# Performance work log

Hardware: AMD Instinct MI355X
Metric: run time of the kernel (lower is better)

The kernel has to match this reference:

```python
import jax, jax.numpy as jnp
import numpy as np

B, S_IMG, S_TXT, D, H, HD, R = 1, 1536, 512, 3072, 24, 128, 32
INNER = H * HD  # 3072
EPS = 1e-5


def svdq_linear(x, W, down, up, b=None):
    # Float reference of SVDQW4A4Linear: quantized base GEMM + SVD low-rank branch.
    y = x @ W.T + (x @ down) @ up
    if b is not None:
        y = y + b
    return y


def rms_norm(x, w):
    # RMSNorm over last dim (dim_head)
    var = jnp.mean(x * x, axis=-1, keepdims=True)
    return x * jax.lax.rsqrt(var + EPS) * w


def apply_rope(x, cos, sin):
    # x: (B, S, H, HD); cos/sin: (S, HD//2), interleaved complex rotation
    b, s, h, d = x.shape
    xr = x.reshape(b, s, h, d // 2, 2)
    x0, x1 = xr[..., 0], xr[..., 1]
    c = cos[None, :, None, :]
    sn = sin[None, :, None, :]
    o0 = x0 * c - x1 * sn
    o1 = x0 * sn + x1 * c
    return jnp.stack([o0, o1], axis=-1).reshape(b, s, h, d)


def setup_inputs() -> dict:
    key = jax.random.key(0)
    ks = jax.random.split(key, 24)
    sc = 0.02
    inp = {
        'hidden_states': jax.random.normal(ks[0], (B, S_IMG, D), jnp.float32),
        'encoder_hidden_states': jax.random.normal(ks[1], (B, S_TXT, D), jnp.float32),
    }
    S = S_IMG + S_TXT
    theta = jax.random.uniform(ks[2], (S, HD // 2), jnp.float32, 0.0, 2.0 * np.pi)
    inp['rope_cos'] = jnp.cos(theta)
    inp['rope_sin'] = jnp.sin(theta)
    inp['qkv_w'] = jax.random.normal(ks[3], (3 * INNER, D), jnp.float32) * sc
    inp['qkv_down'] = jax.random.normal(ks[4], (D, R), jnp.float32) * sc
    inp['qkv_up'] = jax.random.normal(ks[5], (R, 3 * INNER), jnp.float32) * sc
    inp['add_qkv_w'] = jax.random.normal(ks[6], (3 * INNER, D), jnp.float32) * sc
    inp['add_qkv_down'] = jax.random.normal(ks[7], (D, R), jnp.float32) * sc
    inp['add_qkv_up'] = jax.random.normal(ks[8], (R, 3 * INNER), jnp.float32) * sc
    inp['out_w'] = jax.random.normal(ks[9], (D, INNER), jnp.float32) * sc
    inp['out_down'] = jax.random.normal(ks[10], (INNER, R), jnp.float32) * sc
    inp['out_up'] = jax.random.normal(ks[11], (R, D), jnp.float32) * sc
    inp['out_b'] = jnp.zeros((D,), jnp.float32)
    inp['add_out_w'] = jax.random.normal(ks[12], (D, INNER), jnp.float32) * sc
    inp['add_out_down'] = jax.random.normal(ks[13], (INNER, R), jnp.float32) * sc
    inp['add_out_up'] = jax.random.normal(ks[14], (R, D), jnp.float32) * sc
    inp['add_out_b'] = jnp.zeros((D,), jnp.float32)
    inp['norm_q_w'] = jnp.ones((HD,), jnp.float32)
    inp['norm_k_w'] = jnp.ones((HD,), jnp.float32)
    inp['norm_added_q_w'] = jnp.ones((HD,), jnp.float32)
    inp['norm_added_k_w'] = jnp.ones((HD,), jnp.float32)
    return inp


def reference(hidden_states, encoder_hidden_states, rope_cos, rope_sin,
              qkv_w, qkv_down, qkv_up,
              add_qkv_w, add_qkv_down, add_qkv_up,
              out_w, out_down, out_up, out_b,
              add_out_w, add_out_down, add_out_up, add_out_b,
              norm_q_w, norm_k_w, norm_added_q_w, norm_added_k_w):
    seq_txt = encoder_hidden_states.shape[1]

    img_qkv = svdq_linear(hidden_states, qkv_w, qkv_down, qkv_up)
    img_q, img_k, img_v = jnp.split(img_qkv, 3, axis=-1)
    txt_qkv = svdq_linear(encoder_hidden_states, add_qkv_w, add_qkv_down, add_qkv_up)
    txt_q, txt_k, txt_v = jnp.split(txt_qkv, 3, axis=-1)

    def heads(x):
        return x.reshape(x.shape[0], x.shape[1], H, HD)

    img_q, img_k, img_v = heads(img_q), heads(img_k), heads(img_v)
    txt_q, txt_k, txt_v = heads(txt_q), heads(txt_k), heads(txt_v)

    img_q = rms_norm(img_q, norm_q_w)
    img_k = rms_norm(img_k, norm_k_w)
    txt_q = rms_norm(txt_q, norm_added_q_w)
    txt_k = rms_norm(txt_k, norm_added_k_w)

    q = jnp.concatenate([txt_q, img_q], axis=1)  # (B, S, H, HD)
    k = jnp.concatenate([txt_k, img_k], axis=1)
    v = jnp.concatenate([txt_v, img_v], axis=1)

    q = apply_rope(q, rope_cos, rope_sin)
    k = apply_rope(k, rope_cos, rope_sin)

    scale = 1.0 / jnp.sqrt(jnp.asarray(HD, q.dtype))
    scores = jnp.einsum('bqhd,bkhd->bhqk', q, k) * scale
    probs = jax.nn.softmax(scores, axis=-1)
    attn = jnp.einsum('bhqk,bkhd->bqhd', probs, v)
    attn = attn.reshape(attn.shape[0], attn.shape[1], INNER)

    txt_attn = attn[:, :seq_txt, :]
    img_attn = attn[:, seq_txt:, :]

    img_out = svdq_linear(img_attn, out_w, out_down, out_up, out_b)
    txt_out = svdq_linear(txt_attn, add_out_w, add_out_down, add_out_up, add_out_b)
    return (img_out, txt_out)
```

## Files before the change

kernel.cpp:

```cpp
#include <hip/hip_runtime.h>
#include <hip/hip_bf16.h>
#include <stdint.h>

typedef __hip_bfloat16 bf16;
typedef __attribute__((ext_vector_type(8))) short short8;
typedef __attribute__((ext_vector_type(4))) short short4b;
typedef __attribute__((ext_vector_type(4))) float floatx4;

__device__ __forceinline__ short bfs(float x) {
    uint32_t u = __builtin_bit_cast(uint32_t, x);
    u += 0x7FFFu + ((u >> 16) & 1u);
    return (short)(u >> 16);
}
__device__ __forceinline__ float b2f(bf16 x) { return __bfloat162float(x); }

__device__ __forceinline__ void load_lds16(const bf16* g, bf16* l) {
    __builtin_amdgcn_global_load_lds(
        (const __attribute__((address_space(1))) uint32_t*)g,
        (__attribute__((address_space(3))) uint32_t*)l, 16, 0, 0);
}

__global__ __launch_bounds__(256) void cvt_bf16(const float* __restrict__ X,
                                                bf16* __restrict__ Y) {
    const size_t i = ((size_t)blockIdx.x * 256 + threadIdx.x) * 8;
    const float4 v0 = *(const float4*)(X + i);
    const float4 v1 = *(const float4*)(X + i + 4);
    short8 o = { bfs(v0.x), bfs(v0.y), bfs(v0.z), bfs(v0.w),
                 bfs(v1.x), bfs(v1.y), bfs(v1.z), bfs(v1.w) };
    *(short8*)(Y + i) = o;
}

__global__ __launch_bounds__(64) void transposeR(const float* __restrict__ U,
                                                 bf16* __restrict__ UT, int N) {
    const int n = blockIdx.x * 64 + threadIdx.x;
    #pragma unroll
    for (int r = 0; r < 32; ++r)
        UT[(size_t)n * 32 + r] = __float2bfloat16(U[(size_t)r * N + n]);
}

__global__ __launch_bounds__(256) void downproj(const bf16* __restrict__ X,
                                                const float* __restrict__ Dn,
                                                bf16* __restrict__ T, int K) {
    const int m = blockIdx.x;
    const int n = threadIdx.x & 31;
    const int kg = threadIdx.x >> 5;
    const bf16* x = X + (size_t)m * K;
    const int kc = K >> 3;
    float acc = 0.f;
    #pragma unroll 4
    for (int k = kg * kc; k < (kg + 1) * kc; ++k)
        acc += b2f(x[k]) * Dn[(size_t)k * 32 + n];
    __shared__ float red[8][32];
    red[kg][n] = acc;
    __syncthreads();
    if (threadIdx.x < 32) {
        float s = 0.f;
        #pragma unroll
        for (int g = 0; g < 8; ++g) s += red[g][n];
        T[(size_t)m * 32 + n] = __float2bfloat16(s);
    }
}

__global__ __launch_bounds__(256) void gemm128(
    const bf16* __restrict__ A0, const bf16* __restrict__ B0,
    const bf16* __restrict__ T0, const bf16* __restrict__ U0,
    const bf16* __restrict__ A1, const bf16* __restrict__ B1,
    const bf16* __restrict__ T1, const bf16* __restrict__ U1,
    const float* __restrict__ bias0, const float* __restrict__ bias1,
    float* __restrict__ C0, float* __restrict__ C1,
    bf16* __restrict__ Qb, bf16* __restrict__ Kb, bf16* __restrict__ Vb,
    int mtiles0, int N, int K, int sb0, int sb1, int mode)
{
    __shared__ __align__(16) bf16 As[2][128 * 32];
    __shared__ __align__(16) bf16 Bs[2][128 * 32];
    const int tid = threadIdx.x;
    const int lane = tid & 63, w = tid >> 6;
    const int wm = (w >> 1) * 64, wn = (w & 1) * 64;
    const int lr = lane & 15, lq = lane >> 4;

    int bid = blockIdx.y * gridDim.x + blockIdx.x;
    const int cpx = (gridDim.x * gridDim.y) >> 3;
    bid = (bid & 7) * cpx + (bid >> 3);
    const int by = bid / gridDim.x, bx = bid - by * gridDim.x;

    const bool set1 = (by >= mtiles0);
    const int lby = set1 ? (by - mtiles0) : by;
    const int m0 = lby * 128, n0 = bx * 128;
    const bf16* Asel = set1 ? A1 : A0;
    const bf16* Bsel = set1 ? B1 : B0;
    const bf16* Tsel = set1 ? T1 : T0;
    const bf16* Usel = set1 ? U1 : U0;
    const int s_base = set1 ? sb1 : sb0;

    const int ksteps = K >> 5;

    auto stage = [&](int buf, int kt) {
        const bf16 *a_src, *b_src;
        int lda, ldb;
        if (kt < ksteps) {
            a_src = Asel + (size_t)m0 * K + kt * 32; lda = K;
            b_src = Bsel + (size_t)n0 * K + kt * 32; ldb = K;
        } else {
            a_src = Tsel + (size_t)m0 * 32; lda = 32;
            b_src = Usel + (size_t)n0 * 32; ldb = 32;
        }
        bf16* Ad = &As[buf][0];
        bf16* Bd = &Bs[buf][0];
        #pragma unroll
        for (int it = 0; it < 2; ++it) {
            const int c = tid + it * 256;
            const int row = c >> 2, sub = c & 3;
            load_lds16(a_src + (size_t)row * lda + sub * 8, Ad + c * 8);
        }
        #pragma unroll
        for (int it = 0; it < 2; ++it) {
            const int c = tid + it * 256;
            const int row = c >> 2, sub = c & 3;
            load_lds16(b_src + (size_t)row * ldb + sub * 8, Bd + c * 8);
        }
    };

    floatx4 acc[4][4] = {};
    stage(0, 0);
    __syncthreads();
    int cur = 0;
    for (int kt = 0; kt <= ksteps; ++kt) {
        if (kt < ksteps) stage(cur ^ 1, kt + 1);
        const bf16* Ac = &As[cur][0];
        const bf16* Bc = &Bs[cur][0];
        short8 af[4], bfr[4];
        #pragma unroll
        for (int i = 0; i < 4; ++i)
            af[i] = *(const short8*)(Ac + (wm + i * 16 + lr) * 32 + lq * 8);
        #pragma unroll
        for (int j = 0; j < 4; ++j)
            bfr[j] = *(const short8*)(Bc + (wn + j * 16 + lr) * 32 + lq * 8);
        #pragma unroll
        for (int i = 0; i < 4; ++i)
            #pragma unroll
            for (int j = 0; j < 4; ++j)
                acc[i][j] = __builtin_amdgcn_mfma_f32_16x16x32_bf16(
                    af[i], bfr[j], acc[i][j], 0, 0, 0);
        __syncthreads();
        cur ^= 1;
    }

    if (mode == 0) {
        float* Csel = set1 ? C1 : C0;
        const float* bsel = set1 ? bias1 : bias0;
        #pragma unroll
        for (int j = 0; j < 4; ++j) {
            const int col = n0 + wn + j * 16 + lr;
            const float bv = bsel ? bsel[col] : 0.0f;
            #pragma unroll
            for (int i = 0; i < 4; ++i) {
                const int rowb = m0 + wm + i * 16 + lq * 4;
                #pragma unroll
                for (int r = 0; r < 4; ++r)
                    Csel[(size_t)(rowb + r) * N + col] = acc[i][j][r] + bv;
            }
        }
    } else {
        #pragma unroll
        for (int j = 0; j < 4; ++j) {
            const int col = n0 + wn + j * 16 + lr;
            const int which = col / 3072;
            const int cc = col - which * 3072;
            const int hh = cc >> 7, dd = cc & 127;
            #pragma unroll
            for (int i = 0; i < 4; ++i) {
                const int rowb = m0 + wm + i * 16 + lq * 4;
                const int s0 = s_base + rowb;
                if (which == 2) {
                    short4b pv = { bfs(acc[i][j][0]), bfs(acc[i][j][1]),
                                   bfs(acc[i][j][2]), bfs(acc[i][j][3]) };
                    *(short4b*)(Vb + ((size_t)hh * 128 + dd) * 2048 + s0) = pv;
                } else {
                    bf16* dst = (which == 0 ? Qb : Kb)
                              + ((size_t)hh * 2048 + s0) * 128 + dd;
                    #pragma unroll
                    for (int r = 0; r < 4; ++r)
                        dst[(size_t)r * 128] = __float2bfloat16(acc[i][j][r]);
                }
            }
        }
    }
}

__global__ __launch_bounds__(256) void rmsrope(
    bf16* __restrict__ Qb, bf16* __restrict__ Kb,
    const float* __restrict__ cosb, const float* __restrict__ sinb,
    const float* __restrict__ nqw, const float* __restrict__ nkw,
    const float* __restrict__ naqw, const float* __restrict__ nakw)
{
    const int idx = blockIdx.x * 4 + (threadIdx.x >> 6);
    const int i = threadIdx.x & 63;
    const int s = idx & 2047;
    const int h = idx >> 11;
    const float c  = cosb[s * 64 + i];
    const float sn = sinb[s * 64 + i];
    const bool txt = (s < 512);
    const size_t base = ((size_t)h * 2048 + s) * 128;

    {
        __hip_bfloat162* row = (__hip_bfloat162*)(Qb + base);
        __hip_bfloat162 pv = row[i];
        float x0 = b2f(pv.x), x1 = b2f(pv.y);
        float ss = x0 * x0 + x1 * x1;
        #pragma unroll
        for (int m = 1; m < 64; m <<= 1) ss += __shfl_xor(ss, m);
        const float rms = rsqrtf(ss * (1.0f / 128.0f) + 1e-5f);
        const float2 nw = *(const float2*)((txt ? naqw : nqw) + 2 * i);
        const float y0 = x0 * rms * nw.x;
        const float y1 = x1 * rms * nw.y;
        __hip_bfloat162 o;
        o.x = __float2bfloat16(y0 * c - y1 * sn);
        o.y = __float2bfloat16(y0 * sn + y1 * c);
        row[i] = o;
    }
    {
        __hip_bfloat162* row = (__hip_bfloat162*)(Kb + base);
        __hip_bfloat162 pv = row[i];
        float x0 = b2f(pv.x), x1 = b2f(pv.y);
        float ss = x0 * x0 + x1 * x1;
        #pragma unroll
        for (int m = 1; m < 64; m <<= 1) ss += __shfl_xor(ss, m);
        const float rms = rsqrtf(ss * (1.0f / 128.0f) + 1e-5f);
        const float2 nw = *(const float2*)((txt ? nakw : nkw) + 2 * i);
        const float y0 = x0 * rms * nw.x;
        const float y1 = x1 * rms * nw.y;
        __hip_bfloat162 o;
        o.x = __float2bfloat16(y0 * c - y1 * sn);
        o.y = __float2bfloat16(y0 * sn + y1 * c);
        row[i] = o;
    }
}

__global__ __launch_bounds__(256) void attn64(
    const bf16* __restrict__ Qb, const bf16* __restrict__ Kb,
    const bf16* __restrict__ Vb, bf16* __restrict__ attnb)
{
    __shared__ __align__(16) bf16 Ks[64 * 128];
    __shared__ __align__(16) bf16 VsT[128 * 64];
    __shared__ __align__(16) bf16 Ps[4][16 * 64];
    const int tid = threadIdx.x, lane = tid & 63, w = tid >> 6;
    const int lr = lane & 15, lq = lane >> 4;
    const int h = blockIdx.y, q0 = blockIdx.x * 64;
    const float scale = 0.08838834764831845f;

    const bf16* qrow = Qb + ((size_t)h * 2048 + q0 + w * 16 + lr) * 128;
    short8 qf[4];
    #pragma unroll
    for (int ks = 0; ks < 4; ++ks)
        qf[ks] = *(const short8*)(qrow + ks * 32 + lq * 8);

    floatx4 oacc[8] = {};
    float mrow[4] = {-1e30f, -1e30f, -1e30f, -1e30f};
    float lrow[4] = {0.f, 0.f, 0.f, 0.f};

    for (int kt = 0; kt < 32; ++kt) {
        const int kv0 = kt * 64;
        __syncthreads();
        #pragma unroll
        for (int it = 0; it < 4; ++it) {
            const int c = tid + it * 256;
            const int row = c >> 4, cg = (c & 15) ^ (row & 7);
            load_lds16(Kb + ((size_t)h * 2048 + kv0 + row) * 128 + cg * 8,
                       Ks + c * 8);
        }
        #pragma unroll
        for (int it = 0; it < 4; ++it) {
            const int c = tid + it * 256;
            const int row = c >> 3, cg = (c & 7) ^ (row & 7);
            load_lds16(Vb + ((size_t)h * 128 + row) * 2048 + kv0 + cg * 8,
                       VsT + c * 8);
        }
        __syncthreads();

        floatx4 sacc[4] = {};
        __builtin_amdgcn_s_setprio(1);
        #pragma unroll
        for (int ks = 0; ks < 4; ++ks)
            #pragma unroll
            for (int jt = 0; jt < 4; ++jt) {
                const int row = jt * 16 + lr;
                short8 kf = *(const short8*)(
                    Ks + row * 128 + (((ks * 4 + lq) ^ (row & 7)) * 8));
                sacc[jt] = __builtin_amdgcn_mfma_f32_16x16x32_bf16(qf[ks], kf, sacc[jt], 0, 0, 0);
            }
        __builtin_amdgcn_s_setprio(0);

        float alpha_r[4];
        #pragma unroll
        for (int r = 0; r < 4; ++r) {
            float s0 = sacc[0][r] * scale, s1 = sacc[1][r] * scale;
            float s2 = sacc[2][r] * scale, s3 = sacc[3][r] * scale;
            float mx = fmaxf(fmaxf(s0, s1), fmaxf(s2, s3));
            #pragma unroll
            for (int msk = 1; msk < 16; msk <<= 1)
                mx = fmaxf(mx, __shfl_xor(mx, msk));
            const float mn = fmaxf(mrow[r], mx);
            const float al = __expf(mrow[r] - mn);
            s0 = __expf(s0 - mn); s1 = __expf(s1 - mn);
            s2 = __expf(s2 - mn); s3 = __expf(s3 - mn);
            float sum = s0 + s1 + s2 + s3;
            #pragma unroll
            for (int msk = 1; msk < 16; msk <<= 1)
                sum += __shfl_xor(sum, msk);
            lrow[r] = lrow[r] * al + sum;
            mrow[r] = mn;
            alpha_r[r] = al;
            sacc[0][r] = s0; sacc[1][r] = s1; sacc[2][r] = s2; sacc[3][r] = s3;
        }
        #pragma unroll
        for (int nt = 0; nt < 8; ++nt)
            #pragma unroll
            for (int r = 0; r < 4; ++r) oacc[nt][r] *= alpha_r[r];

        #pragma unroll
        for (int jt = 0; jt < 4; ++jt)
            #pragma unroll
            for (int r = 0; r < 4; ++r) {
                const int q = lq * 4 + r;
                const int ir = jt * 16 + lr;
                Ps[w][q * 64 + ((((ir >> 3) ^ (q & 7))) << 3) + (ir & 7)] =
                    __float2bfloat16(sacc[jt][r]);
            }

        short8 pf[2];
        #pragma unroll
        for (int k2 = 0; k2 < 2; ++k2)
            pf[k2] = *(const short8*)(
                &Ps[w][lr * 64 + (((k2 * 4 + lq) ^ (lr & 7)) << 3)]);
        __builtin_amdgcn_s_setprio(1);
        #pragma unroll
        for (int k2 = 0; k2 < 2; ++k2)
            #pragma unroll
            for (int nt = 0; nt < 8; ++nt) {
                const int row = nt * 16 + lr;
                short8 vf = *(const short8*)(
                    VsT + row * 64 + (((k2 * 4 + lq) ^ (row & 7)) * 8));
                oacc[nt] = __builtin_amdgcn_mfma_f32_16x16x32_bf16(pf[k2], vf, oacc[nt], 0, 0, 0);
            }
        __builtin_amdgcn_s_setprio(0);
    }

    float rl[4];
    #pragma unroll
    for (int r = 0; r < 4; ++r) rl[r] = 1.0f / lrow[r];
    #pragma unroll
    for (int nt = 0; nt < 8; ++nt) {
        const int col = h * 128 + nt * 16 + lr;
        #pragma unroll
        for (int r = 0; r < 4; ++r) {
            const int s = q0 + w * 16 + lq * 4 + r;
            attnb[(size_t)s * 3072 + col] = __float2bfloat16(oacc[nt][r] * rl[r]);
        }
    }
}

extern "C" void kernel_launch(void* const* d_in, const int* in_sizes, int n_in,
                              void* d_out, int out_size, void* d_ws, size_t ws_size,
                              hipStream_t stream)
{
    (void)in_sizes; (void)n_in; (void)out_size; (void)ws_size;
    const float* hs        = (const float*)d_in[0];
    const float* ehs       = (const float*)d_in[1];
    const float* rc        = (const float*)d_in[2];
    const float* rs        = (const float*)d_in[3];
    const float* qkv_w     = (const float*)d_in[4];
    const float* qkv_down  = (const float*)d_in[5];
    const float* qkv_up    = (const float*)d_in[6];
    const float* aqkv_w    = (const float*)d_in[7];
    const float* aqkv_down = (const float*)d_in[8];
    const float* aqkv_up   = (const float*)d_in[9];
    const float* out_w     = (const float*)d_in[10];
    const float* out_down  = (const float*)d_in[11];
    const float* out_up    = (const float*)d_in[12];
    const float* out_b     = (const float*)d_in[13];
    const float* aout_w    = (const float*)d_in[14];
    const float* aout_down = (const float*)d_in[15];
    const float* aout_up   = (const float*)d_in[16];
    const float* aout_b    = (const float*)d_in[17];
    const float* nqw  = (const float*)d_in[18];
    const float* nkw  = (const float*)d_in[19];
    const float* naqw = (const float*)d_in[20];
    const float* nakw = (const float*)d_in[21];

    char* ws = (char*)d_ws;
    size_t o = 0;
    bf16* Qb = (bf16*)(ws + o); o += (size_t)24 * 2048 * 128 * 2;
    bf16* Kb = (bf16*)(ws + o); o += (size_t)24 * 2048 * 128 * 2;
    bf16* Vb = (bf16*)(ws + o); o += (size_t)24 * 2048 * 128 * 2;
    bf16* attnb = (bf16*)(ws + o); o += (size_t)2048 * 3072 * 2;
    bf16* Xbi = (bf16*)(ws + o); o += (size_t)1536 * 3072 * 2;
    bf16* Xbt = (bf16*)(ws + o); o += (size_t)512 * 3072 * 2;
    bf16* Wq  = (bf16*)(ws + o); o += (size_t)9216 * 3072 * 2;
    bf16* Waq = (bf16*)(ws + o); o += (size_t)9216 * 3072 * 2;
    bf16* Wo  = Wq;
    bf16* Wao = Wq + (size_t)3072 * 3072;
    bf16* t_img  = (bf16*)(ws + o); o += (size_t)1536 * 32 * 2;
    bf16* t_txt  = (bf16*)(ws + o); o += (size_t)512 * 32 * 2;
    bf16* t2_img = (bf16*)(ws + o); o += (size_t)1536 * 32 * 2;
    bf16* t2_txt = (bf16*)(ws + o); o += (size_t)512 * 32 * 2;
    bf16* upTq  = (bf16*)(ws + o); o += (size_t)9216 * 32 * 2;
    bf16* upTaq = (bf16*)(ws + o); o += (size_t)9216 * 32 * 2;
    bf16* upTo  = (bf16*)(ws + o); o += (size_t)3072 * 32 * 2;
    bf16* upTao = (bf16*)(ws + o); o += (size_t)3072 * 32 * 2;

    cvt_bf16<<<2304, 256, 0, stream>>>(hs, Xbi);
    cvt_bf16<<<768, 256, 0, stream>>>(ehs, Xbt);
    cvt_bf16<<<13824, 256, 0, stream>>>(qkv_w, Wq);
    cvt_bf16<<<13824, 256, 0, stream>>>(aqkv_w, Waq);

    transposeR<<<144, 64, 0, stream>>>(qkv_up, upTq, 9216);
    transposeR<<<144, 64, 0, stream>>>(aqkv_up, upTaq, 9216);
    transposeR<<<48, 64, 0, stream>>>(out_up, upTo, 3072);
    transposeR<<<48, 64, 0, stream>>>(aout_up, upTao, 3072);
    downproj<<<1536, 256, 0, stream>>>(Xbi, qkv_down, t_img, 3072);
    downproj<<<512, 256, 0, stream>>>(Xbt, aqkv_down, t_txt, 3072);

    gemm128<<<dim3(72, 16), 256, 0, stream>>>(
        Xbi, Wq, t_img, upTq,
        Xbt, Waq, t_txt, upTaq,
        nullptr, nullptr, nullptr, nullptr,
        Qb, Kb, Vb, 12, 9216, 3072, 512, 0, 1);

    cvt_bf16<<<4608, 256, 0, stream>>>(out_w, Wo);
    cvt_bf16<<<4608, 256, 0, stream>>>(aout_w, Wao);

    rmsrope<<<12288, 256, 0, stream>>>(Qb, Kb, rc, rs, nqw, nkw, naqw, nakw);

    attn64<<<dim3(32, 24), 256, 0, stream>>>(Qb, Kb, Vb, attnb);

    downproj<<<1536, 256, 0, stream>>>(attnb + (size_t)512 * 3072, out_down, t2_img, 3072);
    downproj<<<512, 256, 0, stream>>>(attnb, aout_down, t2_txt, 3072);

    float* outp = (float*)d_out;
    gemm128<<<dim3(24, 16), 256, 0, stream>>>(
        attnb + (size_t)512 * 3072, Wo, t2_img, upTo,
        attnb,                      Wao, t2_txt, upTao,
        out_b, aout_b, outp, outp + (size_t)1536 * 3072,
        nullptr, nullptr, nullptr, 12, 3072, 3072, 0, 0, 0);
}
```

Before: 953.9 us.

## Widen GEMM K-tile to 64 with swizzled LDS and interleaved staging phases

The GEMM main loop now steps K by 64 instead of 32, which halves the number of loop iterations and barriers. LDS tiles use an XOR swizzle on the column groups to avoid bank conflicts. The next-tile global-to-LDS loads are split into four parts, each interleaved with one row-block of MFMAs and separated by s_barrier/sched_barrier, with setprio raised around the MFMAs. The low-rank buffers are zero-padded to a rank of 64 so the extra LoRA step fits the 64-wide tile, at the cost of doubled LDS usage and some wasted MFMA work on the padding.

```diff
diff --git a/kernel.cpp b/kernel.cpp
--- a/kernel.cpp
+++ b/kernel.cpp
@@ -19,6 +19,9 @@
         (const __attribute__((address_space(1))) uint32_t*)g,
         (__attribute__((address_space(3))) uint32_t*)l, 16, 0, 0);
 }
+
+#define PHASE_BARRIER() do { __builtin_amdgcn_s_barrier(); \
+                             __builtin_amdgcn_sched_barrier(0); } while (0)
 
 __global__ __launch_bounds__(256) void cvt_bf16(const float* __restrict__ X,
                                                 bf16* __restrict__ Y) {
@@ -34,8 +37,10 @@
                                                  bf16* __restrict__ UT, int N) {
     const int n = blockIdx.x * 64 + threadIdx.x;
     #pragma unroll
-    for (int r = 0; r < 32; ++r)
-        UT[(size_t)n * 32 + r] = __float2bfloat16(U[(size_t)r * N + n]);
+    for (int r = 0; r < 32; ++r) {
+        UT[(size_t)n * 64 + r] = __float2bfloat16(U[(size_t)r * N + n]);
+        UT[(size_t)n * 64 + 32 + r] = __float2bfloat16(0.0f);
+    }
 }
 
 __global__ __launch_bounds__(256) void downproj(const bf16* __restrict__ X,
@@ -57,11 +62,12 @@
         float s = 0.f;
         #pragma unroll
         for (int g = 0; g < 8; ++g) s += red[g][n];
-        T[(size_t)m * 32 + n] = __float2bfloat16(s);
-    }
-}
-
-__global__ __launch_bounds__(256) void gemm128(
+        T[(size_t)m * 64 + n] = __float2bfloat16(s);
+        T[(size_t)m * 64 + 32 + n] = __float2bfloat16(0.0f);
+    }
+}
+
+__global__ __launch_bounds__(256) void gemm64k(
     const bf16* __restrict__ A0, const bf16* __restrict__ B0,
     const bf16* __restrict__ T0, const bf16* __restrict__ U0,
     const bf16* __restrict__ A1, const bf16* __restrict__ B1,
@@ -71,8 +77,8 @@
     bf16* __restrict__ Qb, bf16* __restrict__ Kb, bf16* __restrict__ Vb,
     int mtiles0, int N, int K, int sb0, int sb1, int mode)
 {
-    __shared__ __align__(16) bf16 As[2][128 * 32];
-    __shared__ __align__(16) bf16 Bs[2][128 * 32];
+    __shared__ __align__(16) bf16 As[2][128 * 64];
+    __shared__ __align__(16) bf16 Bs[2][128 * 64];
     const int tid = threadIdx.x;
     const int lane = tid & 63, w = tid >> 6;
     const int wm = (w >> 1) * 64, wn = (w & 1) * 64;
@@ -92,57 +98,90 @@
     const bf16* Usel = set1 ? U1 : U0;
     const int s_base = set1 ? sb1 : sb0;
 
-    const int ksteps = K >> 5;
-
-    auto stage = [&](int buf, int kt) {
-        const bf16 *a_src, *b_src;
-        int lda, ldb;
-        if (kt < ksteps) {
-            a_src = Asel + (size_t)m0 * K + kt * 32; lda = K;
-            b_src = Bsel + (size_t)n0 * K + kt * 32; ldb = K;
-        } else {
-            a_src = Tsel + (size_t)m0 * 32; lda = 32;
-            b_src = Usel + (size_t)n0 * 32; ldb = 32;
-        }
-        bf16* Ad = &As[buf][0];
-        bf16* Bd = &Bs[buf][0];
+    const int ksteps = K >> 6;
+
+    auto stageA = [&](int buf, int kt, int part) {
+        const bf16* src; int ld;
+        if (kt < ksteps) { src = Asel + (size_t)m0 * K + kt * 64; ld = K; }
+        else             { src = Tsel + (size_t)m0 * 64;          ld = 64; }
+        bf16* dst = &As[buf][0];
         #pragma unroll
         for (int it = 0; it < 2; ++it) {
-            const int c = tid + it * 256;
-            const int row = c >> 2, sub = c & 3;
-            load_lds16(a_src + (size_t)row * lda + sub * 8, Ad + c * 8);
-        }
+            const int c = tid + part * 512 + it * 256;
+            const int row = c >> 3, cg = (c & 7) ^ (row & 7);
+            load_lds16(src + (size_t)row * ld + cg * 8, dst + c * 8);
+        }
+    };
+    auto stageB = [&](int buf, int kt, int part) {
+        const bf16* src; int ld;
+        if (kt < ksteps) { src = Bsel + (size_t)n0 * K + kt * 64; ld = K; }
+        else             { src = Usel + (size_t)n0 * 64;          ld = 64; }
+        bf16* dst = &Bs[buf][0];
         #pragma unroll
         for (int it = 0; it < 2; ++it) {
-            const int c = tid + it * 256;
-            const int row = c >> 2, sub = c & 3;
-            load_lds16(b_src + (size_t)row * ldb + sub * 8, Bd + c * 8);
+            const int c = tid + part * 512 + it * 256;
+            const int row = c >> 3, cg = (c & 7) ^ (row & 7);
+            load_lds16(src + (size_t)row * ld + cg * 8, dst + c * 8);
         }
     };
 
     floatx4 acc[4][4] = {};
-    stage(0, 0);
+    short8 bfr[4][2];
+
+    stageA(0, 0, 0); stageA(0, 0, 1);
+    stageB(0, 0, 0); stageB(0, 0, 1);
     __syncthreads();
-    int cur = 0;
+
     for (int kt = 0; kt <= ksteps; ++kt) {
-        if (kt < ksteps) stage(cur ^ 1, kt + 1);
-        const bf16* Ac = &As[cur][0];
-        const bf16* Bc = &Bs[cur][0];
-        short8 af[4], bfr[4];
-        #pragma unroll
-        for (int i = 0; i < 4; ++i)
-            af[i] = *(const short8*)(Ac + (wm + i * 16 + lr) * 32 + lq * 8);
-        #pragma unroll
-        for (int j = 0; j < 4; ++j)
-            bfr[j] = *(const short8*)(Bc + (wn + j * 16 + lr) * 32 + lq * 8);
-        #pragma unroll
-        for (int i = 0; i < 4; ++i)
-            #pragma unroll
-            for (int j = 0; j < 4; ++j)
-                acc[i][j] = __builtin_amdgcn_mfma_f32_16x16x32_bf16(
-                    af[i], bfr[j], acc[i][j], 0, 0, 0);
+        const int buf = kt & 1, nbuf = buf ^ 1;
+        const bool more = (kt < ksteps);
+        const bf16* Ac = &As[buf][0];
+        const bf16* Bc = &Bs[buf][0];
+
+        auto readA = [&](int p, short8 af[2]) {
+            const int row = wm + p * 16 + lr;
+            #pragma unroll
+            for (int k2 = 0; k2 < 2; ++k2)
+                af[k2] = *(const short8*)(
+                    Ac + row * 64 + (((k2 * 4 + lq) ^ (row & 7)) << 3));
+        };
+        auto mfmaP = [&](int p, short8 af[2]) {
+            __builtin_amdgcn_s_setprio(1);
+            #pragma unroll
+            for (int k2 = 0; k2 < 2; ++k2)
+                #pragma unroll
+                for (int j = 0; j < 4; ++j)
+                    acc[p][j] = __builtin_amdgcn_mfma_f32_16x16x32_bf16(
+                        af[k2], bfr[j][k2], acc[p][j], 0, 0, 0);
+            __builtin_amdgcn_s_setprio(0);
+        };
+
+        short8 af[2];
+        #pragma unroll
+        for (int j = 0; j < 4; ++j) {
+            const int row = wn + j * 16 + lr;
+            #pragma unroll
+            for (int k2 = 0; k2 < 2; ++k2)
+                bfr[j][k2] = *(const short8*)(
+                    Bc + row * 64 + (((k2 * 4 + lq) ^ (row & 7)) << 3));
+        }
+        readA(0, af);
+        if (more) stageA(nbuf, kt + 1, 0);
+        PHASE_BARRIER();
+        mfmaP(0, af);
+        readA(1, af);
+        if (more) stageA(nbuf, kt + 1, 1);
+        PHASE_BARRIER();
+        mfmaP(1, af);
+        readA(2, af);
+        if (more) stageB(nbuf, kt + 1, 0);
+        PHASE_BARRIER();
+        mfmaP(2, af);
+        readA(3, af);
+        if (more) stageB(nbuf, kt + 1, 1);
+        PHASE_BARRIER();
+        mfmaP(3, af);
         __syncthreads();
-        cur ^= 1;
     }
 
     if (mode == 0) {
@@ -399,14 +438,14 @@
     bf16* Waq = (bf16*)(ws + o); o += (size_t)9216 * 3072 * 2;
     bf16* Wo  = Wq;
     bf16* Wao = Wq + (size_t)3072 * 3072;
-    bf16* t_img  = (bf16*)(ws + o); o += (size_t)1536 * 32 * 2;
-    bf16* t_txt  = (bf16*)(ws + o); o += (size_t)512 * 32 * 2;
-    bf16* t2_img = (bf16*)(ws + o); o += (size_t)1536 * 32 * 2;
-    bf16* t2_txt = (bf16*)(ws + o); o += (size_t)512 * 32 * 2;
-    bf16* upTq  = (bf16*)(ws + o); o += (size_t)9216 * 32 * 2;
-    bf16* upTaq = (bf16*)(ws + o); o += (size_t)9216 * 32 * 2;
-    bf16* upTo  = (bf16*)(ws + o); o += (size_t)3072 * 32 * 2;
-    bf16* upTao = (bf16*)(ws + o); o += (size_t)3072 * 32 * 2;
+    bf16* t_img  = (bf16*)(ws + o); o += (size_t)1536 * 64 * 2;
+    bf16* t_txt  = (bf16*)(ws + o); o += (size_t)512 * 64 * 2;
+    bf16* t2_img = (bf16*)(ws + o); o += (size_t)1536 * 64 * 2;
+    bf16* t2_txt = (bf16*)(ws + o); o += (size_t)512 * 64 * 2;
+    bf16* upTq  = (bf16*)(ws + o); o += (size_t)9216 * 64 * 2;
+    bf16* upTaq = (bf16*)(ws + o); o += (size_t)9216 * 64 * 2;
+    bf16* upTo  = (bf16*)(ws + o); o += (size_t)3072 * 64 * 2;
+    bf16* upTao = (bf16*)(ws + o); o += (size_t)3072 * 64 * 2;
 
     cvt_bf16<<<2304, 256, 0, stream>>>(hs, Xbi);
     cvt_bf16<<<768, 256, 0, stream>>>(ehs, Xbt);
@@ -420,7 +459,7 @@
     downproj<<<1536, 256, 0, stream>>>(Xbi, qkv_down, t_img, 3072);
     downproj<<<512, 256, 0, stream>>>(Xbt, aqkv_down, t_txt, 3072);
 
-    gemm128<<<dim3(72, 16), 256, 0, stream>>>(
+    gemm64k<<<dim3(72, 16), 256, 0, stream>>>(
         Xbi, Wq, t_img, upTq,
         Xbt, Waq, t_txt, upTaq,
         nullptr, nullptr, nullptr, nullptr,
@@ -437,7 +476,7 @@
     downproj<<<512, 256, 0, stream>>>(attnb, aout_down, t2_txt, 3072);
 
     float* outp = (float*)d_out;
-    gemm128<<<dim3(24, 16), 256, 0, stream>>>(
+    gemm64k<<<dim3(24, 16), 256, 0, stream>>>(
         attnb + (size_t)512 * 3072, Wo, t2_img, upTo,
         attnb,                      Wao, t2_txt, upTao,
         out_b, aout_b, outp, outp + (size_t)1536 * 3072,
```

New measurement: 951.1 us. About the same (-0.3%).
